# Performance work log

Hardware: AMD Instinct MI355X
Metric: run time of the kernel (lower is better)

The kernel has to match this reference:

```python
import jax, jax.numpy as jnp
import numpy as np

HOMO_BOOST_THRD = 0.5
HOMO_LOSS_WEIGHT = 100.0
EPS = 1e-8  # F.cosine_similarity default eps

N_NODES = 50000
N_EDGES = 1600000
D_FEAT = 128
N_TARGET = 5000
N_BKD = 500


def setup_inputs() -> dict:
    key = jax.random.key(0)
    k1, k2, k3, k4, k5 = jax.random.split(key, 5)
    edge_index = jax.random.randint(k1, (2, N_EDGES), 0, N_NODES, dtype=jnp.int64 if jax.config.jax_enable_x64 else jnp.int32)
    edge_weights = jax.random.uniform(k2, (N_EDGES,), dtype=jnp.float32)
    x = jax.random.normal(k3, (N_NODES, D_FEAT), dtype=jnp.float32)
    target_nodes = jax.random.randint(k4, (N_TARGET,), 0, N_NODES)
    bkd_nodes = jax.random.randint(k5, (N_BKD,), 0, N_NODES)
    return {"edge_index": edge_index, "edge_weights": edge_weights, "x": x,
            "target_nodes": target_nodes, "bkd_nodes": bkd_nodes}


def reference(edge_index, edge_weights, x, target_nodes, bkd_nodes):
    n = x.shape[0]
    # membership bitmaps replace per-edge python `in set` checks
    is_bkd = jnp.zeros((n,), dtype=bool).at[bkd_nodes].set(True)
    is_tgt = jnp.zeros((n,), dtype=bool).at[target_nodes].set(True)

    u, v = edge_index[0], edge_index[1]
    # dense_to_sparse in the original drops zero-weight edges
    mask = ((is_bkd[u] & is_tgt[v]) | (is_bkd[v] & is_tgt[u])) & (edge_weights != 0)

    xu = x[u]  # [E, d]
    xv = x[v]  # [E, d]
    dot = jnp.sum(xu * xv, axis=-1)
    nu = jnp.maximum(jnp.linalg.norm(xu, axis=-1), EPS)
    nv = jnp.maximum(jnp.linalg.norm(xv, axis=-1), EPS)
    sims = dot / (nu * nv)  # F.cosine_similarity

    per_edge = jnp.maximum(HOMO_BOOST_THRD - sims, 0.0)  # clamp-at-zero branch
    loss = HOMO_LOSS_WEIGHT * jnp.sum(jnp.where(mask, per_edge, 0.0))
    return loss
```

## Files before the change

### kernel.cpp

```cpp
#include <hip/hip_runtime.h>

#define HOMO_BOOST_THRD 0.5f
#define HOMO_LOSS_WEIGHT 100.0f
#define COS_EPS 1e-8f
#define D_FEAT 128
#define EDGE_BLOCK 256
#define EPT 8
#define NWAVES (EDGE_BLOCK / 64)
#define QMAX 256

#define FLAG_WORDS_MAX 4096

__global__ __launch_bounds__(EDGE_BLOCK) void edge_loss_kernel(
        const int* __restrict__ edge_index,
        const float* __restrict__ edge_weights,
        const float* __restrict__ x,
        const int* __restrict__ target_nodes, int n_tgt,
        const int* __restrict__ bkd_nodes, int n_bkd,
        float* __restrict__ partials, int E, int nwords) {
    __shared__ unsigned int sflags[FLAG_WORDS_MAX];
    __shared__ int2 q[QMAX];
    __shared__ int qn;
    __shared__ float wsum[NWAVES];

    uint4* s4 = reinterpret_cast<uint4*>(sflags);
    const int nwords4 = (nwords + 3) >> 2;
    for (int i = threadIdx.x; i < nwords4; i += EDGE_BLOCK)
        s4[i] = make_uint4(0u, 0u, 0u, 0u);
    if (threadIdx.x == 0) qn = 0;
    __syncthreads();

    const int n_tgt4 = n_tgt >> 2;
    const int4* t4 = reinterpret_cast<const int4*>(target_nodes);
    for (int i = threadIdx.x; i < n_tgt4; i += EDGE_BLOCK) {
        int4 nd = t4[i];
        atomicOr(&sflags[nd.x >> 4], 2u << ((nd.x & 15) * 2));
        atomicOr(&sflags[nd.y >> 4], 2u << ((nd.y & 15) * 2));
        atomicOr(&sflags[nd.z >> 4], 2u << ((nd.z & 15) * 2));
        atomicOr(&sflags[nd.w >> 4], 2u << ((nd.w & 15) * 2));
    }
    for (int i = (n_tgt4 << 2) + threadIdx.x; i < n_tgt; i += EDGE_BLOCK) {
        int node = target_nodes[i];
        atomicOr(&sflags[node >> 4], 2u << ((node & 15) * 2));
    }
    const int n_bkd4 = n_bkd >> 2;
    const int4* b4 = reinterpret_cast<const int4*>(bkd_nodes);
    for (int i = threadIdx.x; i < n_bkd4; i += EDGE_BLOCK) {
        int4 nd = b4[i];
        atomicOr(&sflags[nd.x >> 4], 1u << ((nd.x & 15) * 2));
        atomicOr(&sflags[nd.y >> 4], 1u << ((nd.y & 15) * 2));
        atomicOr(&sflags[nd.z >> 4], 1u << ((nd.z & 15) * 2));
        atomicOr(&sflags[nd.w >> 4], 1u << ((nd.w & 15) * 2));
    }
    for (int i = (n_bkd4 << 2) + threadIdx.x; i < n_bkd; i += EDGE_BLOCK) {
        int node = bkd_nodes[i];
        atomicOr(&sflags[node >> 4], 1u << ((node & 15) * 2));
    }
    __syncthreads();

    const int lane = threadIdx.x & 63;
    const int base = (blockIdx.x * EDGE_BLOCK + threadIdx.x) * EPT;
    const bool full = ((blockIdx.x + 1) * EDGE_BLOCK * EPT <= E) && ((E & 3) == 0);

    int us[EPT], vs[EPT];
    if (full) {
        const int4* up = reinterpret_cast<const int4*>(edge_index + base);
        const int4* vp = reinterpret_cast<const int4*>(edge_index + E + base);
        #pragma unroll
        for (int qd = 0; qd < EPT / 4; ++qd) {
            int4 uq = up[qd];
            int4 vq = vp[qd];
            us[qd*4+0] = uq.x; us[qd*4+1] = uq.y; us[qd*4+2] = uq.z; us[qd*4+3] = uq.w;
            vs[qd*4+0] = vq.x; vs[qd*4+1] = vq.y; vs[qd*4+2] = vq.z; vs[qd*4+3] = vq.w;
        }
    } else {
        #pragma unroll
        for (int k = 0; k < EPT; ++k) {
            int e = base + k;
            bool ok = (e < E);
            us[k] = ok ? edge_index[e] : 0;
            vs[k] = ok ? edge_index[E + e] : 0;
        }
    }

    float wval = 0.0f;

    #pragma unroll
    for (int k = 0; k < EPT; ++k) {
        bool valid = full || (base + k < E);
        unsigned fu = (sflags[us[k] >> 4] >> ((us[k] & 15) * 2)) & 3u;
        unsigned fv = (sflags[vs[k] >> 4] >> ((vs[k] & 15) * 2)) & 3u;
        bool m = valid && ((((fu & (fv >> 1)) | (fv & (fu >> 1))) & 1u) != 0);
        bool ovf = false;
        if (m) {
            float w = edge_weights[base + k];
            if (w != 0.0f) {
                int qi = atomicAdd(&qn, 1);
                if (qi < QMAX) q[qi] = make_int2(us[k], vs[k]);
                else ovf = true;
            }
        }
        unsigned long long ob = __ballot(ovf);
        while (ob) {
            int b = __ffsll(ob) - 1;
            ob &= ob - 1;
            int eu = __shfl(us[k], b, 64);
            int ev = __shfl(vs[k], b, 64);
            float2 a = reinterpret_cast<const float2*>(x + (size_t)eu * D_FEAT)[lane];
            float2 c = reinterpret_cast<const float2*>(x + (size_t)ev * D_FEAT)[lane];
            float d = a.x * c.x + a.y * c.y;
            float p = a.x * a.x + a.y * a.y;
            float qq = c.x * c.x + c.y * c.y;
            #pragma unroll
            for (int off = 1; off < 64; off <<= 1) {
                d += __shfl_xor(d, off, 64);
                p += __shfl_xor(p, off, 64);
                qq += __shfl_xor(qq, off, 64);
            }
            if (lane == 0) {
                float nu = fmaxf(sqrtf(p), COS_EPS);
                float nv = fmaxf(sqrtf(qq), COS_EPS);
                wval += fmaxf(HOMO_BOOST_THRD - d / (nu * nv), 0.0f);
            }
        }
    }
    __syncthreads();

    const int wid = threadIdx.x >> 6;
    const int nq  = (qn < QMAX) ? qn : QMAX;

    for (int i = wid * 2; i < nq; i += 2 * NWAVES) {
        bool has1 = (i + 1 < nq);
        int2 e0 = q[i];
        int2 e1 = has1 ? q[i + 1] : e0;

        float2 a0 = reinterpret_cast<const float2*>(x + (size_t)e0.x * D_FEAT)[lane];
        float2 c0 = reinterpret_cast<const float2*>(x + (size_t)e0.y * D_FEAT)[lane];
        float2 a1 = reinterpret_cast<const float2*>(x + (size_t)e1.x * D_FEAT)[lane];
        float2 c1 = reinterpret_cast<const float2*>(x + (size_t)e1.y * D_FEAT)[lane];

        float d0 = a0.x * c0.x + a0.y * c0.y;
        float p0 = a0.x * a0.x + a0.y * a0.y;
        float q0 = c0.x * c0.x + c0.y * c0.y;
        float d1 = a1.x * c1.x + a1.y * c1.y;
        float p1 = a1.x * a1.x + a1.y * a1.y;
        float q1 = c1.x * c1.x + c1.y * c1.y;
        #pragma unroll
        for (int off = 1; off < 64; off <<= 1) {
            d0 += __shfl_xor(d0, off, 64);
            p0 += __shfl_xor(p0, off, 64);
            q0 += __shfl_xor(q0, off, 64);
            d1 += __shfl_xor(d1, off, 64);
            p1 += __shfl_xor(p1, off, 64);
            q1 += __shfl_xor(q1, off, 64);
        }
        if (lane == 0) {
            float nu0 = fmaxf(sqrtf(p0), COS_EPS);
            float nv0 = fmaxf(sqrtf(q0), COS_EPS);
            wval += fmaxf(HOMO_BOOST_THRD - d0 / (nu0 * nv0), 0.0f);
            if (has1) {
                float nu1 = fmaxf(sqrtf(p1), COS_EPS);
                float nv1 = fmaxf(sqrtf(q1), COS_EPS);
                wval += fmaxf(HOMO_BOOST_THRD - d1 / (nu1 * nv1), 0.0f);
            }
        }
    }

    if (lane == 0) wsum[wid] = wval;
    __syncthreads();
    if (threadIdx.x == 0)
        partials[blockIdx.x] = wsum[0] + wsum[1] + wsum[2] + wsum[3];
}

__global__ void reduce_kernel(const float* __restrict__ partials, int n,
                              float* __restrict__ out) {
    __shared__ float wsum[16];
    float s = 0.0f;
    for (int i = threadIdx.x; i < n; i += blockDim.x) s += partials[i];
    #pragma unroll
    for (int off = 32; off > 0; off >>= 1) s += __shfl_down(s, off, 64);
    if ((threadIdx.x & 63) == 0) wsum[threadIdx.x >> 6] = s;
    __syncthreads();
    if (threadIdx.x == 0) {
        float t = 0.0f;
        for (int w = 0; w < (int)(blockDim.x >> 6); ++w) t += wsum[w];
        out[0] = t * HOMO_LOSS_WEIGHT;
    }
}

extern "C" void kernel_launch(void* const* d_in, const int* in_sizes, int n_in,
                              void* d_out, int out_size, void* d_ws, size_t ws_size,
                              hipStream_t stream) {
    const int*   edge_index   = (const int*)  d_in[0];
    const float* edge_weights = (const float*)d_in[1];
    const float* x            = (const float*)d_in[2];
    const int*   target_nodes = (const int*)  d_in[3];
    const int*   bkd_nodes    = (const int*)  d_in[4];

    const int E     = in_sizes[0] / 2;
    const int N     = in_sizes[2] / D_FEAT;
    const int n_tgt = in_sizes[3];
    const int n_bkd = in_sizes[4];

    const int nwords = (N + 15) / 16;
    float* partials = (float*)d_ws;

    const int nblocks = (E + EDGE_BLOCK * EPT - 1) / (EDGE_BLOCK * EPT);
    edge_loss_kernel<<<nblocks, EDGE_BLOCK, 0, stream>>>(
        edge_index, edge_weights, x, target_nodes, n_tgt, bkd_nodes, n_bkd,
        partials, E, nwords);

    reduce_kernel<<<1, 1024, 0, stream>>>(partials, nblocks, (float*)d_out);
}
```

Measured before the change: 13.73 us.

## Use byte-per-node flag table and amortize its build over multiple edge chunks per block

Replaces the 2-bit packed flag words built with shared atomics by a byte-per-node table written with plain stores (target pass, sync, then OR of the backdoor bit). Each block now loops over several edge chunks, so the flag-table build is paid once per several chunks and the grid shrinks to about a third. The cost is roughly 50KB of LDS per block, about three times the old 16KB, which lowers how many blocks fit per CU, plus extra per-chunk barriers and queue resets. Fewer blocks also means less parallelism across the GPU for the edge-scanning part.

```diff
diff --git a/kernel.cpp b/kernel.cpp
--- a/kernel.cpp
+++ b/kernel.cpp
@@ -6,10 +6,12 @@
 #define D_FEAT 128
 #define EDGE_BLOCK 256
 #define EPT 8
+#define CHUNK (EDGE_BLOCK * EPT)
 #define NWAVES (EDGE_BLOCK / 64)
 #define QMAX 256
-
-#define FLAG_WORDS_MAX 4096
+#define CHUNKS_PER_BLOCK 3
+
+#define FLAG_BYTES_MAX 50048
 
 __global__ __launch_bounds__(EDGE_BLOCK) void edge_loss_kernel(
         const int* __restrict__ edge_index,
@@ -17,15 +19,15 @@
         const float* __restrict__ x,
         const int* __restrict__ target_nodes, int n_tgt,
         const int* __restrict__ bkd_nodes, int n_bkd,
-        float* __restrict__ partials, int E, int nwords) {
-    __shared__ unsigned int sflags[FLAG_WORDS_MAX];
+        float* __restrict__ partials, int E, int nchunks, int N) {
+    __shared__ unsigned char sflags[FLAG_BYTES_MAX];
     __shared__ int2 q[QMAX];
     __shared__ int qn;
     __shared__ float wsum[NWAVES];
 
     uint4* s4 = reinterpret_cast<uint4*>(sflags);
-    const int nwords4 = (nwords + 3) >> 2;
-    for (int i = threadIdx.x; i < nwords4; i += EDGE_BLOCK)
+    const int nb16 = (N + 15) >> 4;
+    for (int i = threadIdx.x; i < nb16; i += EDGE_BLOCK)
         s4[i] = make_uint4(0u, 0u, 0u, 0u);
     if (threadIdx.x == 0) qn = 0;
     __syncthreads();
@@ -34,136 +36,132 @@
     const int4* t4 = reinterpret_cast<const int4*>(target_nodes);
     for (int i = threadIdx.x; i < n_tgt4; i += EDGE_BLOCK) {
         int4 nd = t4[i];
-        atomicOr(&sflags[nd.x >> 4], 2u << ((nd.x & 15) * 2));
-        atomicOr(&sflags[nd.y >> 4], 2u << ((nd.y & 15) * 2));
-        atomicOr(&sflags[nd.z >> 4], 2u << ((nd.z & 15) * 2));
-        atomicOr(&sflags[nd.w >> 4], 2u << ((nd.w & 15) * 2));
-    }
-    for (int i = (n_tgt4 << 2) + threadIdx.x; i < n_tgt; i += EDGE_BLOCK) {
-        int node = target_nodes[i];
-        atomicOr(&sflags[node >> 4], 2u << ((node & 15) * 2));
-    }
+        sflags[nd.x] = 2; sflags[nd.y] = 2; sflags[nd.z] = 2; sflags[nd.w] = 2;
+    }
+    for (int i = (n_tgt4 << 2) + threadIdx.x; i < n_tgt; i += EDGE_BLOCK)
+        sflags[target_nodes[i]] = 2;
+    __syncthreads();
+
     const int n_bkd4 = n_bkd >> 2;
     const int4* b4 = reinterpret_cast<const int4*>(bkd_nodes);
     for (int i = threadIdx.x; i < n_bkd4; i += EDGE_BLOCK) {
         int4 nd = b4[i];
-        atomicOr(&sflags[nd.x >> 4], 1u << ((nd.x & 15) * 2));
-        atomicOr(&sflags[nd.y >> 4], 1u << ((nd.y & 15) * 2));
-        atomicOr(&sflags[nd.z >> 4], 1u << ((nd.z & 15) * 2));
-        atomicOr(&sflags[nd.w >> 4], 1u << ((nd.w & 15) * 2));
-    }
-    for (int i = (n_bkd4 << 2) + threadIdx.x; i < n_bkd; i += EDGE_BLOCK) {
-        int node = bkd_nodes[i];
-        atomicOr(&sflags[node >> 4], 1u << ((node & 15) * 2));
-    }
+        sflags[nd.x] |= 1; sflags[nd.y] |= 1; sflags[nd.z] |= 1; sflags[nd.w] |= 1;
+    }
+    for (int i = (n_bkd4 << 2) + threadIdx.x; i < n_bkd; i += EDGE_BLOCK)
+        sflags[bkd_nodes[i]] |= 1;
     __syncthreads();
 
     const int lane = threadIdx.x & 63;
-    const int base = (blockIdx.x * EDGE_BLOCK + threadIdx.x) * EPT;
-    const bool full = ((blockIdx.x + 1) * EDGE_BLOCK * EPT <= E) && ((E & 3) == 0);
-
-    int us[EPT], vs[EPT];
-    if (full) {
-        const int4* up = reinterpret_cast<const int4*>(edge_index + base);
-        const int4* vp = reinterpret_cast<const int4*>(edge_index + E + base);
-        #pragma unroll
-        for (int qd = 0; qd < EPT / 4; ++qd) {
-            int4 uq = up[qd];
-            int4 vq = vp[qd];
-            us[qd*4+0] = uq.x; us[qd*4+1] = uq.y; us[qd*4+2] = uq.z; us[qd*4+3] = uq.w;
-            vs[qd*4+0] = vq.x; vs[qd*4+1] = vq.y; vs[qd*4+2] = vq.z; vs[qd*4+3] = vq.w;
+    const int wid  = threadIdx.x >> 6;
+    float wval = 0.0f;
+
+    for (int chunk = blockIdx.x; chunk < nchunks; chunk += gridDim.x) {
+        const int base = chunk * CHUNK + threadIdx.x * EPT;
+        const bool full = ((chunk + 1) * CHUNK <= E) && ((E & 3) == 0);
+
+        int us[EPT], vs[EPT];
+        if (full) {
+            const int4* up = reinterpret_cast<const int4*>(edge_index + base);
+            const int4* vp = reinterpret_cast<const int4*>(edge_index + E + base);
+            #pragma unroll
+            for (int qd = 0; qd < EPT / 4; ++qd) {
+                int4 uq = up[qd];
+                int4 vq = vp[qd];
+                us[qd*4+0] = uq.x; us[qd*4+1] = uq.y; us[qd*4+2] = uq.z; us[qd*4+3] = uq.w;
+                vs[qd*4+0] = vq.x; vs[qd*4+1] = vq.y; vs[qd*4+2] = vq.z; vs[qd*4+3] = vq.w;
+            }
+        } else {
+            #pragma unroll
+            for (int k = 0; k < EPT; ++k) {
+                int e = base + k;
+                bool ok = (e < E);
+                us[k] = ok ? edge_index[e] : 0;
+                vs[k] = ok ? edge_index[E + e] : 0;
+            }
         }
-    } else {
+
         #pragma unroll
         for (int k = 0; k < EPT; ++k) {
-            int e = base + k;
-            bool ok = (e < E);
-            us[k] = ok ? edge_index[e] : 0;
-            vs[k] = ok ? edge_index[E + e] : 0;
+            bool valid = full || (base + k < E);
+            unsigned fu = sflags[us[k]];
+            unsigned fv = sflags[vs[k]];
+            bool m = valid && ((((fu & (fv >> 1)) | (fv & (fu >> 1))) & 1u) != 0);
+            bool ovf = false;
+            if (m) {
+                float w = edge_weights[base + k];
+                if (w != 0.0f) {
+                    int qi = atomicAdd(&qn, 1);
+                    if (qi < QMAX) q[qi] = make_int2(us[k], vs[k]);
+                    else ovf = true;
+                }
+            }
+            unsigned long long ob = __ballot(ovf);
+            while (ob) {
+                int b = __ffsll(ob) - 1;
+                ob &= ob - 1;
+                int eu = __shfl(us[k], b, 64);
+                int ev = __shfl(vs[k], b, 64);
+                float2 a = reinterpret_cast<const float2*>(x + (size_t)eu * D_FEAT)[lane];
+                float2 c = reinterpret_cast<const float2*>(x + (size_t)ev * D_FEAT)[lane];
+                float d = a.x * c.x + a.y * c.y;
+                float p = a.x * a.x + a.y * a.y;
+                float qq = c.x * c.x + c.y * c.y;
+                #pragma unroll
+                for (int off = 1; off < 64; off <<= 1) {
+                    d += __shfl_xor(d, off, 64);
+                    p += __shfl_xor(p, off, 64);
+                    qq += __shfl_xor(qq, off, 64);
+                }
+                if (lane == 0) {
+                    float nu = fmaxf(sqrtf(p), COS_EPS);
+                    float nv = fmaxf(sqrtf(qq), COS_EPS);
+                    wval += fmaxf(HOMO_BOOST_THRD - d / (nu * nv), 0.0f);
+                }
+            }
         }
-    }
-
-    float wval = 0.0f;
-
-    #pragma unroll
-    for (int k = 0; k < EPT; ++k) {
-        bool valid = full || (base + k < E);
-        unsigned fu = (sflags[us[k] >> 4] >> ((us[k] & 15) * 2)) & 3u;
-        unsigned fv = (sflags[vs[k] >> 4] >> ((vs[k] & 15) * 2)) & 3u;
-        bool m = valid && ((((fu & (fv >> 1)) | (fv & (fu >> 1))) & 1u) != 0);
-        bool ovf = false;
-        if (m) {
-            float w = edge_weights[base + k];
-            if (w != 0.0f) {
-                int qi = atomicAdd(&qn, 1);
-                if (qi < QMAX) q[qi] = make_int2(us[k], vs[k]);
-                else ovf = true;
-            }
-        }
-        unsigned long long ob = __ballot(ovf);
-        while (ob) {
-            int b = __ffsll(ob) - 1;
-            ob &= ob - 1;
-            int eu = __shfl(us[k], b, 64);
-            int ev = __shfl(vs[k], b, 64);
-            float2 a = reinterpret_cast<const float2*>(x + (size_t)eu * D_FEAT)[lane];
-            float2 c = reinterpret_cast<const float2*>(x + (size_t)ev * D_FEAT)[lane];
-            float d = a.x * c.x + a.y * c.y;
-            float p = a.x * a.x + a.y * a.y;
-            float qq = c.x * c.x + c.y * c.y;
+        __syncthreads();
+
+        const int nq = (qn < QMAX) ? qn : QMAX;
+        for (int i = wid * 2; i < nq; i += 2 * NWAVES) {
+            bool has1 = (i + 1 < nq);
+            int2 e0 = q[i];
+            int2 e1 = has1 ? q[i + 1] : e0;
+
+            float2 a0 = reinterpret_cast<const float2*>(x + (size_t)e0.x * D_FEAT)[lane];
+            float2 c0 = reinterpret_cast<const float2*>(x + (size_t)e0.y * D_FEAT)[lane];
+            float2 a1 = reinterpret_cast<const float2*>(x + (size_t)e1.x * D_FEAT)[lane];
+            float2 c1 = reinterpret_cast<const float2*>(x + (size_t)e1.y * D_FEAT)[lane];
+
+            float d0 = a0.x * c0.x + a0.y * c0.y;
+            float p0 = a0.x * a0.x + a0.y * a0.y;
+            float q0 = c0.x * c0.x + c0.y * c0.y;
+            float d1 = a1.x * c1.x + a1.y * c1.y;
+            float p1 = a1.x * a1.x + a1.y * a1.y;
+            float q1 = c1.x * c1.x + c1.y * c1.y;
             #pragma unroll
             for (int off = 1; off < 64; off <<= 1) {
-                d += __shfl_xor(d, off, 64);
-                p += __shfl_xor(p, off, 64);
-                qq += __shfl_xor(qq, off, 64);
+                d0 += __shfl_xor(d0, off, 64);
+                p0 += __shfl_xor(p0, off, 64);
+                q0 += __shfl_xor(q0, off, 64);
+                d1 += __shfl_xor(d1, off, 64);
+                p1 += __shfl_xor(p1, off, 64);
+                q1 += __shfl_xor(q1, off, 64);
             }
             if (lane == 0) {
-                float nu = fmaxf(sqrtf(p), COS_EPS);
-                float nv = fmaxf(sqrtf(qq), COS_EPS);
-                wval += fmaxf(HOMO_BOOST_THRD - d / (nu * nv), 0.0f);
+                float nu0 = fmaxf(sqrtf(p0), COS_EPS);
+                float nv0 = fmaxf(sqrtf(q0), COS_EPS);
+                wval += fmaxf(HOMO_BOOST_THRD - d0 / (nu0 * nv0), 0.0f);
+                if (has1) {
+                    float nu1 = fmaxf(sqrtf(p1), COS_EPS);
+                    float nv1 = fmaxf(sqrtf(q1), COS_EPS);
+                    wval += fmaxf(HOMO_BOOST_THRD - d1 / (nu1 * nv1), 0.0f);
+                }
             }
         }
-    }
-    __syncthreads();
-
-    const int wid = threadIdx.x >> 6;
-    const int nq  = (qn < QMAX) ? qn : QMAX;
-
-    for (int i = wid * 2; i < nq; i += 2 * NWAVES) {
-        bool has1 = (i + 1 < nq);
-        int2 e0 = q[i];
-        int2 e1 = has1 ? q[i + 1] : e0;
-
-        float2 a0 = reinterpret_cast<const float2*>(x + (size_t)e0.x * D_FEAT)[lane];
-        float2 c0 = reinterpret_cast<const float2*>(x + (size_t)e0.y * D_FEAT)[lane];
-        float2 a1 = reinterpret_cast<const float2*>(x + (size_t)e1.x * D_FEAT)[lane];
-        float2 c1 = reinterpret_cast<const float2*>(x + (size_t)e1.y * D_FEAT)[lane];
-
-        float d0 = a0.x * c0.x + a0.y * c0.y;
-        float p0 = a0.x * a0.x + a0.y * a0.y;
-        float q0 = c0.x * c0.x + c0.y * c0.y;
-        float d1 = a1.x * c1.x + a1.y * c1.y;
-        float p1 = a1.x * a1.x + a1.y * a1.y;
-        float q1 = c1.x * c1.x + c1.y * c1.y;
-        #pragma unroll
-        for (int off = 1; off < 64; off <<= 1) {
-            d0 += __shfl_xor(d0, off, 64);
-            p0 += __shfl_xor(p0, off, 64);
-            q0 += __shfl_xor(q0, off, 64);
-            d1 += __shfl_xor(d1, off, 64);
-            p1 += __shfl_xor(p1, off, 64);
-            q1 += __shfl_xor(q1, off, 64);
-        }
-        if (lane == 0) {
-            float nu0 = fmaxf(sqrtf(p0), COS_EPS);
-            float nv0 = fmaxf(sqrtf(q0), COS_EPS);
-            wval += fmaxf(HOMO_BOOST_THRD - d0 / (nu0 * nv0), 0.0f);
-            if (has1) {
-                float nu1 = fmaxf(sqrtf(p1), COS_EPS);
-                float nv1 = fmaxf(sqrtf(q1), COS_EPS);
-                wval += fmaxf(HOMO_BOOST_THRD - d1 / (nu1 * nv1), 0.0f);
-            }
-        }
+        __syncthreads();
+        if (threadIdx.x == 0) qn = 0;
+        __syncthreads();
     }
 
     if (lane == 0) wsum[wid] = wval;
@@ -202,13 +200,14 @@
     const int n_tgt = in_sizes[3];
     const int n_bkd = in_sizes[4];
 
-    const int nwords = (N + 15) / 16;
     float* partials = (float*)d_ws;
 
-    const int nblocks = (E + EDGE_BLOCK * EPT - 1) / (EDGE_BLOCK * EPT);
+    const int nchunks = (E + CHUNK - 1) / CHUNK;
+    const int nblocks = (nchunks + CHUNKS_PER_BLOCK - 1) / CHUNKS_PER_BLOCK;
+
     edge_loss_kernel<<<nblocks, EDGE_BLOCK, 0, stream>>>(
         edge_index, edge_weights, x, target_nodes, n_tgt, bkd_nodes, n_bkd,
-        partials, E, nwords);
+        partials, E, nchunks, N);
 
     reduce_kernel<<<1, 1024, 0, stream>>>(partials, nblocks, (float*)d_out);
 }
```

Measured after the change: 18.31 us. +33.3%, slower.
